# Performance work log

Measured on AMD Instinct MI355X. Metric: run time of the kernel, lower is better.

Reference implementation:

```python
import jax, jax.numpy as jnp
import numpy as np

KERNEL_SIZE = 4
STRIDE = 4


def setup_inputs() -> dict:
    key = jax.random.key(0)
    ks = jax.random.split(key, 5)
    b, l, d, hidden = 32, 8192, 256, 512
    x = jax.random.normal(ks[0], (b, l, d), dtype=jnp.float32)
    We = jax.random.normal(ks[1], (d, hidden), dtype=jnp.float32) * (1.0 / np.sqrt(d))
    be = jax.random.normal(ks[2], (hidden,), dtype=jnp.float32) * 0.01
    Wr = jax.random.normal(ks[3], (hidden, 1), dtype=jnp.float32) * (1.0 / np.sqrt(hidden))
    br = jax.random.normal(ks[4], (1,), dtype=jnp.float32) * 0.01
    return {"x": x, "We": We, "be": be, "Wr": Wr, "br": br}


def reference(x, We, be, Wr, br):
    b, l, d = x.shape
    steps = (l - KERNEL_SIZE) // STRIDE + 1
    # window gather: original loop slices x[:, i*stride : i*stride+stride, :]
    idx = jnp.arange(steps)[:, None] * STRIDE + jnp.arange(STRIDE)[None, :]  # (steps, stride)
    win = x[:, idx, :]  # (b, steps, stride, d)
    h = jnp.tanh(win @ We + be)                      # (b, steps, stride, hidden)
    logits = jnp.squeeze(h @ Wr, -1) + br            # (b, steps, stride)
    w = jax.nn.softmax(jax.nn.sigmoid(logits), axis=-1)
    out = jnp.einsum('bswd,bsw->bsd', win, w)        # softmax-weighted sum over window
    return out
```

## Files before the change

### kernel.cpp

```cpp
#include <hip/hip_runtime.h>
#include <hip/hip_bf16.h>

typedef __attribute__((ext_vector_type(8))) short bf16x8;
typedef __attribute__((ext_vector_type(4))) short short4v;
typedef __attribute__((ext_vector_type(4))) float f32x4;

#define D        256
#define NH       512
#define NT       32
#define KT       8
#define MT       4
#define ROWS_PER_BLOCK 64
#define ROWS_TOTAL (32*8192)

typedef __attribute__((address_space(1))) const void GV;
typedef __attribute__((address_space(3))) void LV;

__device__ __forceinline__ short f2bf(float f) {
    union { float f; unsigned u; } v; v.f = f;
    unsigned r = v.u + 0x7FFFu + ((v.u >> 16) & 1u);
    return (short)(r >> 16);
}
__device__ __forceinline__ float rcp_fast(float x) {
    return __builtin_amdgcn_rcpf(x);
}

__global__ void prepack_B(const float* __restrict__ We, const float* __restrict__ be,
                          const float* __restrict__ Wr,
                          short* __restrict__ Bh, float2* __restrict__ bw,
                          float* __restrict__ Ssum) {
    int i = blockIdx.x * 256 + threadIdx.x;
    int k = i >> 9;
    int n = i & 511;
    int nt = n >> 4, c = n & 15;
    int kt = k >> 5, g = (k >> 3) & 3, j = k & 7;
    int idx = (((nt * 8 + kt) * 64) + (g * 16 + c)) * 8 + j;
    Bh[idx] = f2bf(We[i]);
    if (i < 512) bw[i] = make_float2(2.0f * be[i], Wr[i]);
    if (i == 0) {
        float s = 0.0f;
        for (int t = 0; t < 512; ++t) s += Wr[t];
        Ssum[0] = s;
    }
}

__global__ __launch_bounds__(64, 2) void softpool_main(
    const float* __restrict__ x, const short* __restrict__ Bh,
    const float2* __restrict__ bwg, const float* __restrict__ br,
    const float* __restrict__ Ssum, float* __restrict__ out)
{
    const int lane = threadIdx.x;
    const int c = lane & 15;
    const int g = lane >> 4;
    const long row0 = (long)blockIdx.x * ROWS_PER_BLOCK;

    __shared__ short Bl[2][4096];
    __shared__ float2 bwl[512];

    const short* gB = Bh + lane * 8;

    #define STAGE(buf, ntv) {                                                  \
        const short* _g = gB + (long)(ntv) * 4096;                             \
        _Pragma("unroll")                                                      \
        for (int kk = 0; kk < 8; ++kk)                                         \
            __builtin_amdgcn_global_load_lds((GV*)(_g + kk * 512),             \
                (LV*)&Bl[buf][kk * 512], 16, 0, 0);                            \
    }

    #define VM0 asm volatile("s_waitcnt vmcnt(0)" ::: "memory");

    STAGE(1, 0)

    #pragma unroll
    for (int i = 0; i < 4; ++i) {
        float4 v = ((const float4*)bwg)[lane * 4 + i];
        ((float4*)bwl)[lane * 4 + i] = v;
    }

    bf16x8 a[MT][KT];
    char* Asl = (char*)&Bl[0][0];
    #pragma unroll
    for (int m = 0; m < MT; ++m) {
        #pragma unroll
        for (int half = 0; half < 2; ++half) {
            const float* rb = x + (row0 + m * 16 + half * 8) * D;
            float4 st[8];
            #pragma unroll
            for (int i = 0; i < 8; ++i)
                st[i] = ((const float4*)(rb + i * D))[lane];
            #pragma unroll
            for (int i = 0; i < 8; ++i) {
                const int row = half * 8 + i;
                short4v t;
                t[0] = f2bf(st[i].x); t[1] = f2bf(st[i].y);
                t[2] = f2bf(st[i].z); t[3] = f2bf(st[i].w);
                const int boff = row * 512 + ((lane * 8) ^ ((row & 7) << 4));
                *(short4v*)(Asl + boff) = t;
            }
        }
        #pragma unroll
        for (int kt = 0; kt < KT; ++kt) {
            const int boff = c * 512 + ((kt * 64 + g * 16) ^ ((c & 7) << 4));
            a[m][kt] = *(const bf16x8*)(Asl + boff);
        }
    }

    float lps[MT][4];
    #pragma unroll
    for (int m = 0; m < MT; ++m)
        #pragma unroll
        for (int r = 0; r < 4; ++r) lps[m][r] = 0.0f;

    f32x4 accA[MT], accB[MT];

    #define MFMA_(buf, accv) {                                                 \
        _Pragma("unroll")                                                      \
        for (int m = 0; m < MT; ++m)                                           \
            _Pragma("unroll")                                                  \
            for (int r = 0; r < 4; ++r) accv[m][r] = 0.0f;                     \
        _Pragma("unroll")                                                      \
        for (int kt = 0; kt < KT; ++kt) {                                      \
            bf16x8 b = *(const bf16x8*)&Bl[buf][kt * 512 + lane * 8];          \
            _Pragma("unroll")                                                  \
            for (int m = 0; m < MT; ++m)                                       \
                accv[m] = __builtin_amdgcn_mfma_f32_16x16x32_bf16(             \
                             a[m][kt], b, accv[m], 0, 0, 0);                   \
        }                                                                      \
    }

    #define TANH_(accv, ntv) {                                                 \
        float2 bwv = bwl[(ntv) * 16 + c];                                      \
        _Pragma("unroll")                                                      \
        for (int m = 0; m < MT; ++m)                                           \
            _Pragma("unroll")                                                  \
            for (int r = 0; r < 4; ++r) {                                      \
                float z = __builtin_fmaf(accv[m][r], 2.0f, bwv.x);             \
                float e = __expf(z);                                           \
                float rr = rcp_fast(e + 1.0f);                                 \
                lps[m][r] = __builtin_fmaf(bwv.y, rr, lps[m][r]);              \
            }                                                                  \
    }

    VM0
    STAGE(0, 1)
    MFMA_(1, accA)
    VM0

    for (int it = 0; it < 15; ++it) {
        STAGE(1, 2 * it + 2)
        MFMA_(0, accB)
        TANH_(accA, 2 * it)
        VM0
        STAGE(0, 2 * it + 3)
        MFMA_(1, accA)
        TANH_(accB, 2 * it + 1)
        VM0
    }
    MFMA_(0, accB)
    TANH_(accA, 30)
    TANH_(accB, 31)

    const float brv = br[0];
    const float S = Ssum[0];
    #pragma unroll
    for (int m = 0; m < MT; ++m) {
        float l0 = lps[m][0], l1 = lps[m][1], l2 = lps[m][2], l3 = lps[m][3];
        #pragma unroll
        for (int off = 1; off < 16; off <<= 1) {
            l0 += __shfl_xor(l0, off, 64);
            l1 += __shfl_xor(l1, off, 64);
            l2 += __shfl_xor(l2, off, 64);
            l3 += __shfl_xor(l3, off, 64);
        }
        float g0 = S - 2.0f * l0 + brv;
        float g1 = S - 2.0f * l1 + brv;
        float g2 = S - 2.0f * l2 + brv;
        float g3 = S - 2.0f * l3 + brv;
        float s0 = rcp_fast(1.0f + __expf(-g0));
        float s1 = rcp_fast(1.0f + __expf(-g1));
        float s2 = rcp_fast(1.0f + __expf(-g2));
        float s3 = rcp_fast(1.0f + __expf(-g3));
        float e0 = __expf(s0), e1 = __expf(s1), e2 = __expf(s2), e3 = __expf(s3);
        float inv = rcp_fast(e0 + e1 + e2 + e3);
        float w0 = e0 * inv, w1 = e1 * inv, w2 = e2 * inv, w3 = e3 * inv;

        const long wrow = row0 + m * 16 + g * 4;
        const long W = wrow >> 2;
        const float* xw = x + wrow * D + c * 4;
        float* op = out + W * D + c * 4;
        #pragma unroll
        for (int q = 0; q < 4; ++q) {
            float4 r0 = *(const float4*)(xw + 0 * D + q * 64);
            float4 r1 = *(const float4*)(xw + 1 * D + q * 64);
            float4 r2 = *(const float4*)(xw + 2 * D + q * 64);
            float4 r3 = *(const float4*)(xw + 3 * D + q * 64);
            float4 oo;
            oo.x = w0 * r0.x + w1 * r1.x + w2 * r2.x + w3 * r3.x;
            oo.y = w0 * r0.y + w1 * r1.y + w2 * r2.y + w3 * r3.y;
            oo.z = w0 * r0.z + w1 * r1.z + w2 * r2.z + w3 * r3.z;
            oo.w = w0 * r0.w + w1 * r1.w + w2 * r2.w + w3 * r3.w;
            *(float4*)(op + q * 64) = oo;
        }
    }
}

extern "C" void kernel_launch(void* const* d_in, const int* in_sizes, int n_in,
                              void* d_out, int out_size, void* d_ws, size_t ws_size,
                              hipStream_t stream) {
    const float* x  = (const float*)d_in[0];
    const float* We = (const float*)d_in[1];
    const float* be = (const float*)d_in[2];
    const float* Wr = (const float*)d_in[3];
    const float* br = (const float*)d_in[4];
    float* out = (float*)d_out;

    char* ws = (char*)d_ws;
    short*  Bh   = (short*)ws;
    float2* bwp  = (float2*)(ws + 262144);
    float*  Ssum = (float*)(ws + 262144 + 4096);

    prepack_B<<<NH * D / 256, 256, 0, stream>>>(We, be, Wr, Bh, bwp, Ssum);

    const int blocks = ROWS_TOTAL / ROWS_PER_BLOCK;
    softpool_main<<<blocks, 64, 0, stream>>>(x, Bh, bwp, br, Ssum, out);
}
```

Measured before the change: 140.7 us.

## Share staged weight tiles across two waves per block with cooperative loads

Each block now holds two waves covering 128 rows. Each wave loads half of every bf16 weight tile into shared LDS, and `__syncthreads` barriers keep the two halves in step. This halves the weight-tile traffic from L2 per row, which was large because each 64-row wave re-streamed the full 256 KB weight matrix. To save registers it drops the dual-accumulator scheme so occupancy can rise. The cost is barrier stalls and less overlap between MFMA and the tanh epilogue within a wave.

```diff
diff --git a/kernel.cpp b/kernel.cpp
--- a/kernel.cpp
+++ b/kernel.cpp
@@ -10,7 +10,7 @@
 #define NT       32
 #define KT       8
 #define MT       4
-#define ROWS_PER_BLOCK 64
+#define ROWS_PER_BLOCK 128
 #define ROWS_TOTAL (32*8192)
 
 typedef __attribute__((address_space(1))) const void GV;
@@ -44,41 +44,40 @@
     }
 }
 
-__global__ __launch_bounds__(64, 2) void softpool_main(
+__global__ __launch_bounds__(128, 3) void softpool_main(
     const float* __restrict__ x, const short* __restrict__ Bh,
     const float2* __restrict__ bwg, const float* __restrict__ br,
     const float* __restrict__ Ssum, float* __restrict__ out)
 {
-    const int lane = threadIdx.x;
+    const int tid  = threadIdx.x;
+    const int wave = tid >> 6;
+    const int lane = tid & 63;
     const int c = lane & 15;
     const int g = lane >> 4;
-    const long row0 = (long)blockIdx.x * ROWS_PER_BLOCK;
+    const long row0 = (long)blockIdx.x * ROWS_PER_BLOCK + (long)wave * 64;
 
     __shared__ short Bl[2][4096];
     __shared__ float2 bwl[512];
 
-    const short* gB = Bh + lane * 8;
+    #pragma unroll
+    for (int i = 0; i < 2; ++i)
+        ((float4*)bwl)[tid * 2 + i] = ((const float4*)bwg)[tid * 2 + i];
+
+    const int kt0 = wave * 4;
+    const short* gB = Bh + kt0 * 512 + lane * 8;
 
     #define STAGE(buf, ntv) {                                                  \
         const short* _g = gB + (long)(ntv) * 4096;                             \
         _Pragma("unroll")                                                      \
-        for (int kk = 0; kk < 8; ++kk)                                         \
+        for (int kk = 0; kk < 4; ++kk)                                         \
             __builtin_amdgcn_global_load_lds((GV*)(_g + kk * 512),             \
-                (LV*)&Bl[buf][kk * 512], 16, 0, 0);                            \
+                (LV*)&Bl[buf][(kt0 + kk) * 512], 16, 0, 0);                    \
     }
 
     #define VM0 asm volatile("s_waitcnt vmcnt(0)" ::: "memory");
 
-    STAGE(1, 0)
-
-    #pragma unroll
-    for (int i = 0; i < 4; ++i) {
-        float4 v = ((const float4*)bwg)[lane * 4 + i];
-        ((float4*)bwl)[lane * 4 + i] = v;
-    }
-
     bf16x8 a[MT][KT];
-    char* Asl = (char*)&Bl[0][0];
+    char* Asl = (char*)&Bl[wave][0];
     #pragma unroll
     for (int m = 0; m < MT; ++m) {
         #pragma unroll
@@ -111,54 +110,57 @@
         #pragma unroll
         for (int r = 0; r < 4; ++r) lps[m][r] = 0.0f;
 
-    f32x4 accA[MT], accB[MT];
-
-    #define MFMA_(buf, accv) {                                                 \
+    f32x4 acc[MT];
+
+    #define MFMA_(buf) {                                                       \
         _Pragma("unroll")                                                      \
         for (int m = 0; m < MT; ++m)                                           \
             _Pragma("unroll")                                                  \
-            for (int r = 0; r < 4; ++r) accv[m][r] = 0.0f;                     \
+            for (int r = 0; r < 4; ++r) acc[m][r] = 0.0f;                      \
         _Pragma("unroll")                                                      \
         for (int kt = 0; kt < KT; ++kt) {                                      \
             bf16x8 b = *(const bf16x8*)&Bl[buf][kt * 512 + lane * 8];          \
             _Pragma("unroll")                                                  \
             for (int m = 0; m < MT; ++m)                                       \
-                accv[m] = __builtin_amdgcn_mfma_f32_16x16x32_bf16(             \
-                             a[m][kt], b, accv[m], 0, 0, 0);                   \
+                acc[m] = __builtin_amdgcn_mfma_f32_16x16x32_bf16(              \
+                             a[m][kt], b, acc[m], 0, 0, 0);                    \
         }                                                                      \
     }
 
-    #define TANH_(accv, ntv) {                                                 \
+    #define TANH_(ntv) {                                                       \
         float2 bwv = bwl[(ntv) * 16 + c];                                      \
         _Pragma("unroll")                                                      \
         for (int m = 0; m < MT; ++m)                                           \
             _Pragma("unroll")                                                  \
             for (int r = 0; r < 4; ++r) {                                      \
-                float z = __builtin_fmaf(accv[m][r], 2.0f, bwv.x);             \
+                float z = __builtin_fmaf(acc[m][r], 2.0f, bwv.x);              \
                 float e = __expf(z);                                           \
                 float rr = rcp_fast(e + 1.0f);                                 \
                 lps[m][r] = __builtin_fmaf(bwv.y, rr, lps[m][r]);              \
             }                                                                  \
     }
 
-    VM0
-    STAGE(0, 1)
-    MFMA_(1, accA)
-    VM0
+    __syncthreads();
+
+    STAGE(0, 0)
+    VM0; __syncthreads();
+    STAGE(1, 1)
+    MFMA_(0)
+    TANH_(0)
+    VM0; __syncthreads();
 
     for (int it = 0; it < 15; ++it) {
-        STAGE(1, 2 * it + 2)
-        MFMA_(0, accB)
-        TANH_(accA, 2 * it)
-        VM0
-        STAGE(0, 2 * it + 3)
-        MFMA_(1, accA)
-        TANH_(accB, 2 * it + 1)
-        VM0
-    }
-    MFMA_(0, accB)
-    TANH_(accA, 30)
-    TANH_(accB, 31)
+        STAGE(0, 2 * it + 2)
+        MFMA_(1)
+        TANH_(2 * it + 1)
+        VM0; __syncthreads();
+        STAGE(1, 2 * it + 3)
+        MFMA_(0)
+        TANH_(2 * it + 2)
+        VM0; __syncthreads();
+    }
+    MFMA_(1)
+    TANH_(31)
 
     const float brv = br[0];
     const float S = Ssum[0];
@@ -222,5 +224,5 @@
     prepack_B<<<NH * D / 256, 256, 0, stream>>>(We, be, Wr, Bh, bwp, Ssum);
 
     const int blocks = ROWS_TOTAL / ROWS_PER_BLOCK;
-    softpool_main<<<blocks, 64, 0, stream>>>(x, Bh, bwp, br, Ssum, out);
-}
+    softpool_main<<<blocks, 128, 0, stream>>>(x, Bh, bwp, br, Ssum, out);
+}
```

Result: slower. 279.1 us (+98.4%).
